# Optimization experiments

Hardware: AMD Instinct MI355X
Metric: run time of the kernel (lower is better)

The kernel has to match this reference:

```python
import jax, jax.numpy as jnp
import numpy as np

TOP_K = 4  # num_experts_per_tok


def setup_inputs() -> dict:
    key = jax.random.key(0)
    ks = jax.random.split(key, 7)
    B, S, H, E, I = 1, 1024, 1024, 16, 2880
    scale_h = 1.0 / np.sqrt(H)
    scale_i = 1.0 / np.sqrt(I)
    return {
        "hidden_states": jax.random.normal(ks[0], (B, S, H), jnp.float32),
        "gate_w": jax.random.normal(ks[1], (E, H), jnp.float32) * scale_h,
        "gate_b": jax.random.normal(ks[2], (E,), jnp.float32) * 0.01,
        "gate_up_proj": jax.random.normal(ks[3], (E, H, 2 * I), jnp.float32) * scale_h,
        "gate_up_proj_bias": jax.random.normal(ks[4], (E, 2 * I), jnp.float32) * 0.01,
        "down_proj": jax.random.normal(ks[5], (E, I, H), jnp.float32) * scale_i,
        "down_proj_bias": jax.random.normal(ks[6], (E, H), jnp.float32) * 0.01,
    }


def reference(hidden_states, gate_w, gate_b, gate_up_proj, gate_up_proj_bias,
              down_proj, down_proj_bias):
    B, S, H = hidden_states.shape
    E = gate_w.shape[0]
    I = down_proj.shape[1]
    x = hidden_states.reshape(-1, H)  # [T, H]
    T = x.shape[0]

    # Router: top-k logits, softmax over selected logits only
    router_logits = x @ gate_w.T + gate_b          # [T, E]
    top_vals, top_idx = jax.lax.top_k(router_logits, TOP_K)
    routing_weights = jax.nn.softmax(top_vals, axis=-1)  # [T, K]

    # Combine matrix: C[t, e] = routing weight of expert e for token t (0 if unselected)
    C = jnp.zeros((T, E), x.dtype).at[jnp.arange(T)[:, None], top_idx].add(routing_weights)

    # Dense per-expert MLP (reference computes all experts, combine masks unselected)
    gu = jnp.einsum('th,ehf->tef', x, gate_up_proj) + gate_up_proj_bias[None]  # [T, E, 2I]
    gate, up = gu[..., :I], gu[..., I:]
    inter = jax.nn.silu(gate) * up                                            # [T, E, I]
    expert_out = jnp.einsum('tei,eih->teh', inter, down_proj) + down_proj_bias[None]  # [T, E, H]
    out = jnp.einsum('teh,te->th', expert_out, C)                             # [T, H]

    return out.reshape(B, S, H), router_logits
```

## Files before the change

### kernel.cpp

```cpp
#include <hip/hip_runtime.h>
#include <hip/hip_bf16.h>
#include <stdint.h>

#define T_TOK 1024
#define HDIM  1024
#define NEXP  16
#define IDIM  2880
#define GU_COLS (2*IDIM)
#define TOPK  4

using short4v  = __attribute__((ext_vector_type(4))) short;
using short8   = __attribute__((ext_vector_type(8))) short;
using ushort4v = __attribute__((ext_vector_type(4))) unsigned short;
using f32x4    = __attribute__((ext_vector_type(4))) float;

__device__ __forceinline__ unsigned short f2b(float f) {
    union { float f; unsigned u; } x; x.f = f;
    unsigned r = x.u + 0x7FFFu + ((x.u >> 16) & 1u);
    return (unsigned short)(r >> 16);
}

typedef const __attribute__((address_space(1))) unsigned int* gas1_t;
typedef __attribute__((address_space(3))) unsigned int* las3_t;
__device__ __forceinline__ void gload16(const void* g, void* l) {
    __builtin_amdgcn_global_load_lds((gas1_t)g, (las3_t)l, 16, 0, 0);
}

__global__ __launch_bounds__(256) void router_kernel(
    const float* __restrict__ x, const float* __restrict__ gw,
    const float* __restrict__ gb, float* __restrict__ logits_out,
    int* __restrict__ counts, int* __restrict__ lists, float* __restrict__ wts,
    unsigned short* __restrict__ xb, float* __restrict__ out)
{
    int t = blockIdx.x;
    int tid = threadIdx.x;
    const float* xr = x + (size_t)t * HDIM;
    {
        float4 v = *(const float4*)(xr + tid * 4);
        ushort4v b; b.x = f2b(v.x); b.y = f2b(v.y); b.z = f2b(v.z); b.w = f2b(v.w);
        *(ushort4v*)(xb + (size_t)t * HDIM + tid * 4) = b;
        float4 z = make_float4(0.f, 0.f, 0.f, 0.f);
        *(float4*)(out + (size_t)t * HDIM + tid * 4) = z;
    }
    int e = tid >> 4;
    int l16 = tid & 15;
    const float* wr = gw + (size_t)e * HDIM;
    float p = 0.f;
    for (int h = l16; h < HDIM; h += 16) p += xr[h] * wr[h];
    p += __shfl_xor(p, 8);
    p += __shfl_xor(p, 4);
    p += __shfl_xor(p, 2);
    p += __shfl_xor(p, 1);
    __shared__ float sl[NEXP];
    if (l16 == 0) {
        float v = p + gb[e];
        sl[e] = v;
        logits_out[t * NEXP + e] = v;
    }
    __syncthreads();
    if (tid == 0) {
        float v[NEXP];
#pragma unroll
        for (int i = 0; i < NEXP; ++i) v[i] = sl[i];
        int idx[TOPK]; float tv[TOPK];
        unsigned used = 0;
#pragma unroll
        for (int k = 0; k < TOPK; ++k) {
            float best = -__builtin_inff(); int bi = 0;
#pragma unroll
            for (int i = 0; i < NEXP; ++i)
                if (!((used >> i) & 1u) && v[i] > best) { best = v[i]; bi = i; }
            used |= 1u << bi; idx[k] = bi; tv[k] = best;
        }
        float m = tv[0];
        float ex[TOPK], s = 0.f;
#pragma unroll
        for (int k = 0; k < TOPK; ++k) { ex[k] = expf(tv[k] - m); s += ex[k]; }
#pragma unroll
        for (int k = 0; k < TOPK; ++k) {
            float w = ex[k] / s;
            int slot = atomicAdd(&counts[idx[k]], 1);
            lists[idx[k] * T_TOK + slot] = t;
            wts[idx[k] * T_TOK + slot] = w;
        }
    }
}

__global__ void offsets_kernel(const int* __restrict__ counts, int* __restrict__ offsets)
{
    if (threadIdx.x == 0) {
        int o = 0;
        for (int e = 0; e < NEXP; ++e) { offsets[e] = o; o += counts[e]; }
        offsets[NEXP] = o;
    }
}

__global__ __launch_bounds__(512) void gu_kernel(
    const unsigned short* __restrict__ xb, const float* __restrict__ gup,
    const float* __restrict__ gub, const int* __restrict__ counts,
    const int* __restrict__ offsets, const int* __restrict__ lists,
    unsigned short* __restrict__ inter)
{
    int bid = blockIdx.x;
    int nt = bid % 45;
    int t2 = bid / 45;
    int e  = t2 & 15;
    int mt = t2 >> 4;
    int ne = counts[e];
    if (mt * 256 >= ne) return;

    int tid = threadIdx.x;
    int wave = tid >> 6, lane = tid & 63;
    int l16 = lane & 15, lq = lane >> 4;
    int wm = wave >> 1, wn = wave & 1;

    __shared__ int tokid[256];
    __shared__ unsigned short As[256 * 64];
    __shared__ unsigned short Bs[128 * 64];

    if (tid < 256) {
        int slot = mt * 256 + tid;
        tokid[tid] = (slot < ne) ? lists[e * T_TOK + slot] : lists[e * T_TOK];
    }
    __syncthreads();

    const float* gup_e = gup + (size_t)e * HDIM * GU_COLS;

    int at = tid - 256;
    const unsigned short* asrc[8];
    if (tid >= 256) {
#pragma unroll
        for (int i = 0; i < 8; ++i) {
            int s = at + i * 256;
            int row = s >> 3, c = s & 7;
            asrc[i] = xb + (size_t)tokid[row] * HDIM + ((c ^ (row & 7)) * 8);
        }
    }
    int nb = tid & 15, kb = tid >> 4;
    const float* bsrcg[2];
    if (tid < 256) {
#pragma unroll
        for (int t = 0; t < 2; ++t) {
            int n0 = (nb + t * 16) * 4;
            int is_up = (n0 >> 5) & 1;
            int cw = (n0 & 31) + ((n0 >> 6) << 5);
            size_t gcol = (is_up ? (size_t)IDIM : 0) + (size_t)nt * 64 + cw;
            bsrcg[t] = gup_e + (size_t)(kb * 4) * GU_COLS + gcol;
        }
    }

    f32x4 acc[4][4];
#pragma unroll
    for (int i = 0; i < 4; ++i)
#pragma unroll
        for (int f = 0; f < 4; ++f) acc[i][f] = (f32x4){0.f, 0.f, 0.f, 0.f};

    float4 br[2][4];
    if (tid < 256) {
#pragma unroll
        for (int t = 0; t < 2; ++t)
#pragma unroll
            for (int k = 0; k < 4; ++k)
                br[t][k] = *(const float4*)(bsrcg[t] + (size_t)k * GU_COLS);
    }

    for (int kk = 0; kk < HDIM; kk += 64) {
        __syncthreads();
        if (tid >= 256) {
#pragma unroll
            for (int i = 0; i < 8; ++i)
                gload16(asrc[i] + kk, As + ((size_t)(at + i * 256)) * 8);
        } else {
#pragma unroll
            for (int t = 0; t < 2; ++t)
#pragma unroll
                for (int j = 0; j < 4; ++j) {
                    int n = (nb + t * 16) * 4 + j;
                    int slot = kb ^ (n & 15);
                    ushort4v b;
                    b.x = f2b((&br[t][0].x)[j]); b.y = f2b((&br[t][1].x)[j]);
                    b.z = f2b((&br[t][2].x)[j]); b.w = f2b((&br[t][3].x)[j]);
                    *(ushort4v*)&Bs[n * 64 + slot * 4] = b;
                }
        }
        __syncthreads();
        if (tid < 256 && kk + 64 < HDIM) {
#pragma unroll
            for (int t = 0; t < 2; ++t)
#pragma unroll
                for (int k = 0; k < 4; ++k)
                    br[t][k] = *(const float4*)(bsrcg[t] + (size_t)(kk + 64 + k) * GU_COLS);
        }
        __builtin_amdgcn_s_setprio(1);
#pragma unroll
        for (int ks = 0; ks < 2; ++ks) {
            short8 a[4], b[4];
#pragma unroll
            for (int i = 0; i < 4; ++i) {
                int row = wm * 64 + i * 16 + l16;
                int q = ks * 4 + lq;
                a[i] = *(const short8*)&As[row * 64 + ((q ^ (row & 7)) * 8)];
            }
#pragma unroll
            for (int f = 0; f < 4; ++f) {
                int n = wn * 64 + f * 16 + l16;
                int u0 = (ks * 8 + lq * 2) ^ l16;
                int u1 = (ks * 8 + lq * 2 + 1) ^ l16;
                short4v h0 = *(const short4v*)&Bs[n * 64 + u0 * 4];
                short4v h1 = *(const short4v*)&Bs[n * 64 + u1 * 4];
                b[f] = __builtin_shufflevector(h0, h1, 0, 1, 2, 3, 4, 5, 6, 7);
            }
#pragma unroll
            for (int i = 0; i < 4; ++i)
#pragma unroll
                for (int f = 0; f < 4; ++f)
                    acc[i][f] = __builtin_amdgcn_mfma_f32_16x16x32_bf16(a[i], b[f], acc[i][f], 0, 0, 0);
        }
        __builtin_amdgcn_s_setprio(0);
    }

    int off = offsets[e];
    const float* gbe = gub + (size_t)e * GU_COLS;
#pragma unroll
    for (int j = 0; j < 2; ++j) {
        int cw = wn * 32 + j * 16 + l16;
        float bg = gbe[nt * 64 + cw];
        float bu = gbe[IDIM + nt * 64 + cw];
#pragma unroll
        for (int i = 0; i < 4; ++i)
#pragma unroll
            for (int r = 0; r < 4; ++r) {
                int row = wm * 64 + i * 16 + lq * 4 + r;
                int slot = mt * 256 + row;
                if (slot < ne) {
                    float g = acc[i][j][r] + bg;
                    float u = acc[i][j + 2][r] + bu;
                    float sg = g / (1.f + expf(-g));
                    inter[(size_t)(off + slot) * IDIM + nt * 64 + cw] = f2b(sg * u);
                }
            }
    }
}

__global__ __launch_bounds__(512) void down_kernel(
    const unsigned short* __restrict__ inter, const float* __restrict__ dw,
    const float* __restrict__ db, const int* __restrict__ counts,
    const int* __restrict__ offsets, const int* __restrict__ lists,
    const float* __restrict__ wts, float* __restrict__ out)
{
    int bid = blockIdx.x;
    int ht = bid & 7;
    int t2 = bid >> 3;
    int e  = t2 & 15;
    int mt = t2 >> 4;
    int ne = counts[e];
    if (mt * 256 >= ne) return;

    int tid = threadIdx.x;
    int wave = tid >> 6, lane = tid & 63;
    int l16 = lane & 15, lq = lane >> 4;
    int wm = wave >> 1, wn = wave & 1;

    __shared__ int tokid[256];
    __shared__ float twt[256];
    __shared__ unsigned short As[256 * 64];
    __shared__ unsigned short Bs[128 * 64];

    int off = offsets[e];
    if (tid < 256) {
        int slot = mt * 256 + tid;
        tokid[tid] = (slot < ne) ? lists[e * T_TOK + slot] : -1;
        twt[tid]   = (slot < ne) ? wts[e * T_TOK + slot] : 0.f;
    }
    __syncthreads();

    const float* dw_e = dw + (size_t)e * IDIM * HDIM;

    int at = tid - 256;
    const unsigned short* asrc[8];
    if (tid >= 256) {
#pragma unroll
        for (int i = 0; i < 8; ++i) {
            int s = at + i * 256;
            int row = s >> 3, c = s & 7;
            int slotr = mt * 256 + row; if (slotr >= ne) slotr = ne - 1;
            asrc[i] = inter + (size_t)(off + slotr) * IDIM + ((c ^ (row & 7)) * 8);
        }
    }
    int nb = tid & 15, kb = tid >> 4;
    const float* bsrcg[2];
    if (tid < 256) {
#pragma unroll
        for (int t = 0; t < 2; ++t)
            bsrcg[t] = dw_e + (size_t)(kb * 4) * HDIM + ht * 128 + (nb + t * 16) * 4;
    }

    f32x4 acc[4][4];
#pragma unroll
    for (int i = 0; i < 4; ++i)
#pragma unroll
        for (int f = 0; f < 4; ++f) acc[i][f] = (f32x4){0.f, 0.f, 0.f, 0.f};

    float4 br[2][4];
    if (tid < 256) {
#pragma unroll
        for (int t = 0; t < 2; ++t)
#pragma unroll
            for (int k = 0; k < 4; ++k)
                br[t][k] = *(const float4*)(bsrcg[t] + (size_t)k * HDIM);
    }

    for (int kk = 0; kk < IDIM; kk += 64) {
        __syncthreads();
        if (tid >= 256) {
#pragma unroll
            for (int i = 0; i < 8; ++i)
                gload16(asrc[i] + kk, As + ((size_t)(at + i * 256)) * 8);
        } else {
#pragma unroll
            for (int t = 0; t < 2; ++t)
#pragma unroll
                for (int j = 0; j < 4; ++j) {
                    int n = (nb + t * 16) * 4 + j;
                    int slot = kb ^ (n & 15);
                    ushort4v b;
                    b.x = f2b((&br[t][0].x)[j]); b.y = f2b((&br[t][1].x)[j]);
                    b.z = f2b((&br[t][2].x)[j]); b.w = f2b((&br[t][3].x)[j]);
                    *(ushort4v*)&Bs[n * 64 + slot * 4] = b;
                }
        }
        __syncthreads();
        if (tid < 256 && kk + 64 < IDIM) {
#pragma unroll
            for (int t = 0; t < 2; ++t)
#pragma unroll
                for (int k = 0; k < 4; ++k)
                    br[t][k] = *(const float4*)(bsrcg[t] + (size_t)(kk + 64 + k) * HDIM);
        }
        __builtin_amdgcn_s_setprio(1);
#pragma unroll
        for (int ks = 0; ks < 2; ++ks) {
            short8 a[4], b[4];
#pragma unroll
            for (int i = 0; i < 4; ++i) {
                int row = wm * 64 + i * 16 + l16;
                int q = ks * 4 + lq;
                a[i] = *(const short8*)&As[row * 64 + ((q ^ (row & 7)) * 8)];
            }
#pragma unroll
            for (int f = 0; f < 4; ++f) {
                int n = wn * 64 + f * 16 + l16;
                int u0 = (ks * 8 + lq * 2) ^ l16;
                int u1 = (ks * 8 + lq * 2 + 1) ^ l16;
                short4v h0 = *(const short4v*)&Bs[n * 64 + u0 * 4];
                short4v h1 = *(const short4v*)&Bs[n * 64 + u1 * 4];
                b[f] = __builtin_shufflevector(h0, h1, 0, 1, 2, 3, 4, 5, 6, 7);
            }
#pragma unroll
            for (int i = 0; i < 4; ++i)
#pragma unroll
                for (int f = 0; f < 4; ++f)
                    acc[i][f] = __builtin_amdgcn_mfma_f32_16x16x32_bf16(a[i], b[f], acc[i][f], 0, 0, 0);
        }
        __builtin_amdgcn_s_setprio(0);
    }

    const float* db_e = db + (size_t)e * HDIM;
#pragma unroll
    for (int f = 0; f < 4; ++f) {
        int h = ht * 128 + wn * 64 + f * 16 + l16;
        float bias = db_e[h];
#pragma unroll
        for (int i = 0; i < 4; ++i)
#pragma unroll
            for (int r = 0; r < 4; ++r) {
                int row = wm * 64 + i * 16 + lq * 4 + r;
                int tk = tokid[row];
                if (tk >= 0)
                    atomicAdd(out + (size_t)tk * HDIM + h, twt[row] * (acc[i][f][r] + bias));
            }
    }
}

extern "C" void kernel_launch(void* const* d_in, const int* in_sizes, int n_in,
                              void* d_out, int out_size, void* d_ws, size_t ws_size,
                              hipStream_t stream)
{
    const float* x   = (const float*)d_in[0];
    const float* gw  = (const float*)d_in[1];
    const float* gb  = (const float*)d_in[2];
    const float* gup = (const float*)d_in[3];
    const float* gub = (const float*)d_in[4];
    const float* dw  = (const float*)d_in[5];
    const float* db  = (const float*)d_in[6];

    float* out        = (float*)d_out;
    float* logits_out = out + (size_t)T_TOK * HDIM;

    char* ws = (char*)d_ws;
    int*   counts  = (int*)(ws + 0);
    int*   offsets = (int*)(ws + 256);
    int*   lists   = (int*)(ws + 512);
    float* wts     = (float*)(ws + 512 + 65536);
    unsigned short* xb    = (unsigned short*)(ws + 131584);
    unsigned short* inter = (unsigned short*)(ws + 2228736);

    hipMemsetAsync(counts, 0, 64, stream);

    router_kernel<<<T_TOK, 256, 0, stream>>>(x, gw, gb, logits_out, counts, lists, wts, xb, out);
    offsets_kernel<<<1, 64, 0, stream>>>(counts, offsets);
    gu_kernel<<<4 * NEXP * 45, 512, 0, stream>>>(xb, gup, gub, counts, offsets, lists, inter);
    down_kernel<<<4 * NEXP * 8, 512, 0, stream>>>(inter, dw, db, counts, offsets, lists, wts, out);
}
```

Measured before the change: 346.9 us.

## Split-K down projection, all threads load A and B tiles, new B swizzle

The down-projection kernel is split four ways along the intermediate dimension, giving four times as many blocks. Partial sums are combined through the existing atomic adds, and only the first split adds the bias. Both GEMM kernels stop dedicating half the threads to each operand: every thread now issues both the async A loads and one B float4 group. The register prefetch of B is dropped, the B LDS swizzle becomes one 16-byte read instead of two 8-byte reads, and launch bounds ask for higher occupancy. This trades the removed B prefetch and extra atomic traffic for better load balance, more parallelism in the down pass and fewer LDS instructions.

Result: slower. 368.6 us (+6.3%).

```diff
diff --git a/kernel.cpp b/kernel.cpp
--- a/kernel.cpp
+++ b/kernel.cpp
@@ -9,7 +9,6 @@
 #define GU_COLS (2*IDIM)
 #define TOPK  4
 
-using short4v  = __attribute__((ext_vector_type(4))) short;
 using short8   = __attribute__((ext_vector_type(8))) short;
 using ushort4v = __attribute__((ext_vector_type(4))) unsigned short;
 using f32x4    = __attribute__((ext_vector_type(4))) float;
@@ -95,7 +94,7 @@
     }
 }
 
-__global__ __launch_bounds__(512) void gu_kernel(
+__global__ __launch_bounds__(512, 4) void gu_kernel(
     const unsigned short* __restrict__ xb, const float* __restrict__ gup,
     const float* __restrict__ gub, const int* __restrict__ counts,
     const int* __restrict__ offsets, const int* __restrict__ lists,
@@ -126,71 +125,49 @@
 
     const float* gup_e = gup + (size_t)e * HDIM * GU_COLS;
 
-    int at = tid - 256;
-    const unsigned short* asrc[8];
-    if (tid >= 256) {
-#pragma unroll
-        for (int i = 0; i < 8; ++i) {
-            int s = at + i * 256;
-            int row = s >> 3, c = s & 7;
-            asrc[i] = xb + (size_t)tokid[row] * HDIM + ((c ^ (row & 7)) * 8);
-        }
-    }
-    int nb = tid & 15, kb = tid >> 4;
-    const float* bsrcg[2];
-    if (tid < 256) {
-#pragma unroll
-        for (int t = 0; t < 2; ++t) {
-            int n0 = (nb + t * 16) * 4;
-            int is_up = (n0 >> 5) & 1;
-            int cw = (n0 & 31) + ((n0 >> 6) << 5);
-            size_t gcol = (is_up ? (size_t)IDIM : 0) + (size_t)nt * 64 + cw;
-            bsrcg[t] = gup_e + (size_t)(kb * 4) * GU_COLS + gcol;
-        }
-    }
+    const unsigned short* asrc[4];
+#pragma unroll
+    for (int i = 0; i < 4; ++i) {
+        int s = tid + i * 512;
+        int row = s >> 3, c = s & 7;
+        asrc[i] = xb + (size_t)tokid[row] * HDIM + ((c ^ (row & 7)) * 8);
+    }
+    int nb = tid & 15, kb = (tid >> 4) & 15, bh = tid >> 8;
+    int g = nb + bh * 16;
+    int n0 = g * 4;
+    int is_up = (n0 >> 5) & 1;
+    int cwb = (n0 & 31) + ((n0 >> 6) << 5);
+    const float* bsrc = gup_e + (size_t)(kb * 4) * GU_COLS
+                      + (is_up ? (size_t)IDIM : 0) + (size_t)nt * 64 + cwb;
 
     f32x4 acc[4][4];
 #pragma unroll
     for (int i = 0; i < 4; ++i)
 #pragma unroll
         for (int f = 0; f < 4; ++f) acc[i][f] = (f32x4){0.f, 0.f, 0.f, 0.f};
-
-    float4 br[2][4];
-    if (tid < 256) {
-#pragma unroll
-        for (int t = 0; t < 2; ++t)
-#pragma unroll
-            for (int k = 0; k < 4; ++k)
-                br[t][k] = *(const float4*)(bsrcg[t] + (size_t)k * GU_COLS);
-    }
 
     for (int kk = 0; kk < HDIM; kk += 64) {
         __syncthreads();
-        if (tid >= 256) {
-#pragma unroll
-            for (int i = 0; i < 8; ++i)
-                gload16(asrc[i] + kk, As + ((size_t)(at + i * 256)) * 8);
-        } else {
-#pragma unroll
-            for (int t = 0; t < 2; ++t)
-#pragma unroll
-                for (int j = 0; j < 4; ++j) {
-                    int n = (nb + t * 16) * 4 + j;
-                    int slot = kb ^ (n & 15);
-                    ushort4v b;
-                    b.x = f2b((&br[t][0].x)[j]); b.y = f2b((&br[t][1].x)[j]);
-                    b.z = f2b((&br[t][2].x)[j]); b.w = f2b((&br[t][3].x)[j]);
-                    *(ushort4v*)&Bs[n * 64 + slot * 4] = b;
-                }
+#pragma unroll
+        for (int i = 0; i < 4; ++i)
+            gload16(asrc[i] + kk, As + ((size_t)(tid + i * 512)) * 8);
+        {
+            const float* sp = bsrc + (size_t)kk * GU_COLS;
+            float4 r0 = *(const float4*)(sp);
+            float4 r1 = *(const float4*)(sp + GU_COLS);
+            float4 r2 = *(const float4*)(sp + 2 * GU_COLS);
+            float4 r3 = *(const float4*)(sp + 3 * GU_COLS);
+#pragma unroll
+            for (int j = 0; j < 4; ++j) {
+                int n = n0 + j;
+                int slot = kb ^ ((n & 7) << 1);
+                ushort4v b;
+                b.x = f2b((&r0.x)[j]); b.y = f2b((&r1.x)[j]);
+                b.z = f2b((&r2.x)[j]); b.w = f2b((&r3.x)[j]);
+                *(ushort4v*)&Bs[n * 64 + slot * 4] = b;
+            }
         }
         __syncthreads();
-        if (tid < 256 && kk + 64 < HDIM) {
-#pragma unroll
-            for (int t = 0; t < 2; ++t)
-#pragma unroll
-                for (int k = 0; k < 4; ++k)
-                    br[t][k] = *(const float4*)(bsrcg[t] + (size_t)(kk + 64 + k) * GU_COLS);
-        }
         __builtin_amdgcn_s_setprio(1);
 #pragma unroll
         for (int ks = 0; ks < 2; ++ks) {
@@ -204,11 +181,8 @@
 #pragma unroll
             for (int f = 0; f < 4; ++f) {
                 int n = wn * 64 + f * 16 + l16;
-                int u0 = (ks * 8 + lq * 2) ^ l16;
-                int u1 = (ks * 8 + lq * 2 + 1) ^ l16;
-                short4v h0 = *(const short4v*)&Bs[n * 64 + u0 * 4];
-                short4v h1 = *(const short4v*)&Bs[n * 64 + u1 * 4];
-                b[f] = __builtin_shufflevector(h0, h1, 0, 1, 2, 3, 4, 5, 6, 7);
+                int u = (ks * 8 + lq * 2) ^ ((n & 7) << 1);
+                b[f] = *(const short8*)&Bs[n * 64 + u * 4];
             }
 #pragma unroll
             for (int i = 0; i < 4; ++i)
@@ -233,28 +207,31 @@
                 int row = wm * 64 + i * 16 + lq * 4 + r;
                 int slot = mt * 256 + row;
                 if (slot < ne) {
-                    float g = acc[i][j][r] + bg;
-                    float u = acc[i][j + 2][r] + bu;
-                    float sg = g / (1.f + expf(-g));
-                    inter[(size_t)(off + slot) * IDIM + nt * 64 + cw] = f2b(sg * u);
+                    float gv = acc[i][j][r] + bg;
+                    float uv = acc[i][j + 2][r] + bu;
+                    float sg = gv / (1.f + expf(-gv));
+                    inter[(size_t)(off + slot) * IDIM + nt * 64 + cw] = f2b(sg * uv);
                 }
             }
     }
 }
 
-__global__ __launch_bounds__(512) void down_kernel(
+__global__ __launch_bounds__(512, 4) void down_kernel(
     const unsigned short* __restrict__ inter, const float* __restrict__ dw,
     const float* __restrict__ db, const int* __restrict__ counts,
     const int* __restrict__ offsets, const int* __restrict__ lists,
     const float* __restrict__ wts, float* __restrict__ out)
 {
     int bid = blockIdx.x;
-    int ht = bid & 7;
-    int t2 = bid >> 3;
-    int e  = t2 & 15;
-    int mt = t2 >> 4;
+    int ht  = bid & 7;
+    int e   = (bid >> 3) & 15;
+    int ksp = (bid >> 7) & 3;
+    int mt  = bid >> 9;
     int ne = counts[e];
     if (mt * 256 >= ne) return;
+
+    int k0   = ksp * 768;
+    int kend = (k0 + 768 < IDIM) ? (k0 + 768) : IDIM;
 
     int tid = threadIdx.x;
     int wave = tid >> 6, lane = tid & 63;
@@ -276,24 +253,18 @@
 
     const float* dw_e = dw + (size_t)e * IDIM * HDIM;
 
-    int at = tid - 256;
-    const unsigned short* asrc[8];
-    if (tid >= 256) {
-#pragma unroll
-        for (int i = 0; i < 8; ++i) {
-            int s = at + i * 256;
-            int row = s >> 3, c = s & 7;
-            int slotr = mt * 256 + row; if (slotr >= ne) slotr = ne - 1;
-            asrc[i] = inter + (size_t)(off + slotr) * IDIM + ((c ^ (row & 7)) * 8);
-        }
-    }
-    int nb = tid & 15, kb = tid >> 4;
-    const float* bsrcg[2];
-    if (tid < 256) {
-#pragma unroll
-        for (int t = 0; t < 2; ++t)
-            bsrcg[t] = dw_e + (size_t)(kb * 4) * HDIM + ht * 128 + (nb + t * 16) * 4;
-    }
+    const unsigned short* asrc[4];
+#pragma unroll
+    for (int i = 0; i < 4; ++i) {
+        int s = tid + i * 512;
+        int row = s >> 3, c = s & 7;
+        int slotr = mt * 256 + row; if (slotr >= ne) slotr = ne - 1;
+        asrc[i] = inter + (size_t)(off + slotr) * IDIM + ((c ^ (row & 7)) * 8);
+    }
+    int nb = tid & 15, kb = (tid >> 4) & 15, bh = tid >> 8;
+    int g = nb + bh * 16;
+    int n0 = g * 4;
+    const float* bsrc = dw_e + (size_t)(kb * 4) * HDIM + ht * 128 + n0;
 
     f32x4 acc[4][4];
 #pragma unroll
@@ -301,42 +272,28 @@
 #pragma unroll
         for (int f = 0; f < 4; ++f) acc[i][f] = (f32x4){0.f, 0.f, 0.f, 0.f};
 
-    float4 br[2][4];
-    if (tid < 256) {
-#pragma unroll
-        for (int t = 0; t < 2; ++t)
-#pragma unroll
-            for (int k = 0; k < 4; ++k)
-                br[t][k] = *(const float4*)(bsrcg[t] + (size_t)k * HDIM);
-    }
-
-    for (int kk = 0; kk < IDIM; kk += 64) {
+    for (int kk = k0; kk < kend; kk += 64) {
         __syncthreads();
-        if (tid >= 256) {
-#pragma unroll
-            for (int i = 0; i < 8; ++i)
-                gload16(asrc[i] + kk, As + ((size_t)(at + i * 256)) * 8);
-        } else {
-#pragma unroll
-            for (int t = 0; t < 2; ++t)
-#pragma unroll
-                for (int j = 0; j < 4; ++j) {
-                    int n = (nb + t * 16) * 4 + j;
-                    int slot = kb ^ (n & 15);
-                    ushort4v b;
-                    b.x = f2b((&br[t][0].x)[j]); b.y = f2b((&br[t][1].x)[j]);
-                    b.z = f2b((&br[t][2].x)[j]); b.w = f2b((&br[t][3].x)[j]);
-                    *(ushort4v*)&Bs[n * 64 + slot * 4] = b;
-                }
+#pragma unroll
+        for (int i = 0; i < 4; ++i)
+            gload16(asrc[i] + kk, As + ((size_t)(tid + i * 512)) * 8);
+        {
+            const float* sp = bsrc + (size_t)kk * HDIM;
+            float4 r0 = *(const float4*)(sp);
+            float4 r1 = *(const float4*)(sp + HDIM);
+            float4 r2 = *(const float4*)(sp + 2 * HDIM);
+            float4 r3 = *(const float4*)(sp + 3 * HDIM);
+#pragma unroll
+            for (int j = 0; j < 4; ++j) {
+                int n = n0 + j;
+                int slot = kb ^ ((n & 7) << 1);
+                ushort4v b;
+                b.x = f2b((&r0.x)[j]); b.y = f2b((&r1.x)[j]);
+                b.z = f2b((&r2.x)[j]); b.w = f2b((&r3.x)[j]);
+                *(ushort4v*)&Bs[n * 64 + slot * 4] = b;
+            }
         }
         __syncthreads();
-        if (tid < 256 && kk + 64 < IDIM) {
-#pragma unroll
-            for (int t = 0; t < 2; ++t)
-#pragma unroll
-                for (int k = 0; k < 4; ++k)
-                    br[t][k] = *(const float4*)(bsrcg[t] + (size_t)(kk + 64 + k) * HDIM);
-        }
         __builtin_amdgcn_s_setprio(1);
 #pragma unroll
         for (int ks = 0; ks < 2; ++ks) {
@@ -350,11 +307,8 @@
 #pragma unroll
             for (int f = 0; f < 4; ++f) {
                 int n = wn * 64 + f * 16 + l16;
-                int u0 = (ks * 8 + lq * 2) ^ l16;
-                int u1 = (ks * 8 + lq * 2 + 1) ^ l16;
-                short4v h0 = *(const short4v*)&Bs[n * 64 + u0 * 4];
-                short4v h1 = *(const short4v*)&Bs[n * 64 + u1 * 4];
-                b[f] = __builtin_shufflevector(h0, h1, 0, 1, 2, 3, 4, 5, 6, 7);
+                int u = (ks * 8 + lq * 2) ^ ((n & 7) << 1);
+                b[f] = *(const short8*)&Bs[n * 64 + u * 4];
             }
 #pragma unroll
             for (int i = 0; i < 4; ++i)
@@ -369,7 +323,7 @@
 #pragma unroll
     for (int f = 0; f < 4; ++f) {
         int h = ht * 128 + wn * 64 + f * 16 + l16;
-        float bias = db_e[h];
+        float bias = (ksp == 0) ? db_e[h] : 0.f;
 #pragma unroll
         for (int i = 0; i < 4; ++i)
 #pragma unroll
@@ -410,5 +364,5 @@
     router_kernel<<<T_TOK, 256, 0, stream>>>(x, gw, gb, logits_out, counts, lists, wts, xb, out);
     offsets_kernel<<<1, 64, 0, stream>>>(counts, offsets);
     gu_kernel<<<4 * NEXP * 45, 512, 0, stream>>>(xb, gup, gub, counts, offsets, lists, inter);
-    down_kernel<<<4 * NEXP * 8, 512, 0, stream>>>(inter, dw, db, counts, offsets, lists, wts, out);
-}
+    down_kernel<<<4 * 4 * NEXP * 8, 512, 0, stream>>>(inter, dw, db, counts, offsets, lists, wts, out);
+}
```
